# Kernel optimization log

Hardware: AMD Instinct MI355X
Metric: run time of the kernel (lower is better)

## Reference

```python
import jax, jax.numpy as jnp
import numpy as np


def setup_inputs() -> dict:
    key = jax.random.key(0)
    B, F, H, W, C_out = 8, 64, 128, 128, 32
    V = H * W                     # grid vertices
    E = 3 * V                     # edges; flattened connectivity has 6V entries -> degree 6
    F2 = F // 2
    dim_channel = 6 * F2          # 192
    mid = dim_channel // 2        # 96
    out_ch = 2 * C_out            # 64
    k1, k2, k3, k4 = jax.random.split(key, 4)
    features = jax.random.normal(k1, (B, F, E), dtype=jnp.float32)
    # each vertex appears exactly 6 times in the flattened connectivity
    conn_flat = jax.random.permutation(k2, jnp.tile(jnp.arange(V, dtype=jnp.int32), 6))
    connectivity = conn_flat.reshape(E, 2)
    W1 = jax.random.normal(k3, (dim_channel, mid), dtype=jnp.float32) / np.sqrt(dim_channel)
    b1 = jnp.zeros((mid,), dtype=jnp.float32)
    W2 = jax.random.normal(k4, (mid, out_ch), dtype=jnp.float32) / np.sqrt(mid)
    b2 = jnp.zeros((out_ch,), dtype=jnp.float32)
    return {"features": features, "connectivity": connectivity,
            "output_dim": (H, W, C_out), "W1": W1, "b1": b1, "W2": W2, "b2": b2}


def _occurrence_rank(edges):
    # occ[i] = number of j < i with edges[j] == edges[i] (matches the serial
    # images_index bookkeeping in the torch loop). Stable argsort groups equal
    # vertices while preserving original order within a group.
    n = edges.shape[0]
    order = jnp.argsort(edges)            # stable by default in jax
    sorted_e = edges[order]
    first = jnp.searchsorted(sorted_e, sorted_e, side='left')
    rank_sorted = (jnp.arange(n) - first).astype(jnp.int32)
    return jnp.zeros(n, dtype=jnp.int32).at[order].set(rank_sorted)


def reference(features, connectivity, output_dim, W1, b1, W2, b2):
    B, F, E = features.shape
    H, Wd, C_out = int(output_dim[0]), int(output_dim[1]), int(output_dim[2])
    V = H * Wd
    F2 = F // 2
    edges = connectivity.reshape(-1)                      # [2E]
    # [B, F, E] -> [B, E, F] -> [B, 2E, F/2]: one half-feature per edge endpoint
    mesh = jnp.transpose(features, (0, 2, 1)).reshape(B, 2 * E, F2)
    occ = _occurrence_rank(edges)                         # slot per endpoint, 0..5
    # scatter half-features into [B, V, 6, F/2]; (vertex, slot) pairs are unique
    img = jnp.zeros((B, V, 6, F2), features.dtype).at[:, edges, occ, :].set(mesh)
    x = img.reshape(B, H, Wd, 6 * F2).transpose(0, 3, 1, 2)   # [B, 6*F/2, H, W]
    # 1x1 ConvTranspose2d == pointwise GEMM (torch weight layout [in, out, 1, 1])
    y = jax.nn.relu(jnp.einsum('bihw,io->bohw', x, W1) + b1[None, :, None, None])
    out = jax.nn.relu(jnp.einsum('bihw,io->bohw', y, W2) + b2[None, :, None, None])
    return out
```

## Files before the change

### kernel.cpp

```cpp
#include <hip/hip_runtime.h>
#include <hip/hip_bf16.h>
#include <stdint.h>

namespace {
constexpr int Bb   = 8;
constexpr int Ff   = 64;
constexpr int Ee   = 49152;
constexpr int Vv   = 16384;
constexpr int F2   = 32;
constexpr int TWOE = 2 * Ee;
constexpr int MID  = 96;
constexpr int OUTC = 64;
}

typedef __attribute__((ext_vector_type(8))) short bf16x8;
typedef __attribute__((ext_vector_type(4))) float f32x4;
typedef __attribute__((ext_vector_type(4))) unsigned int u32x4;

__global__ void prep_misc(const float* __restrict__ W1, const float* __restrict__ W2,
                          __hip_bfloat16* __restrict__ w1f, __hip_bfloat16* __restrict__ w2f,
                          int* __restrict__ cnt) {
    int tid = blockIdx.x * 256 + threadIdx.x;
    if (tid < Vv) cnt[tid] = 0;
    if (tid < 18432) {
        int j = tid & 7, l = (tid >> 3) & 63, ft = tid >> 9;
        int kk = ft / 6, nt = ft - kk * 6;
        int k = kk * 32 + (l >> 4) * 8 + j;
        int n = nt * 16 + (l & 15);
        w1f[tid] = __float2bfloat16(W1[k * MID + n]);
    } else if (tid < 24576) {
        int t2 = tid - 18432;
        int j = t2 & 7, l = (t2 >> 3) & 63, ft = t2 >> 9;
        int kk = ft >> 2, nt = ft & 3;
        int k = kk * 32 + (l >> 4) * 8 + j;
        int n = nt * 16 + (l & 15);
        w2f[t2] = __float2bfloat16(W2[k * OUTC + n]);
    }
}

__global__ void bucket_fill(const int* __restrict__ conn, int* __restrict__ cnt,
                            int* __restrict__ buckets) {
    int i = blockIdx.x * 256 + threadIdx.x;
    if (i >= TWOE) return;
    int v = conn[i];
    int pos = atomicAdd(&cnt[v], 1);
    if (pos < 6) buckets[v * 6 + pos] = i;
}

__global__ void sort6_inv(const int* __restrict__ buckets, int* __restrict__ dest) {
    int v = blockIdx.x * 256 + threadIdx.x;
    if (v >= Vv) return;
    int a[6];
#pragma unroll
    for (int k = 0; k < 6; ++k) a[k] = buckets[v * 6 + k];
#define CSWAP(x, y) { int lo = min(a[x], a[y]); int hi = max(a[x], a[y]); a[x] = lo; a[y] = hi; }
    CSWAP(1, 2) CSWAP(4, 5) CSWAP(0, 2) CSWAP(3, 5) CSWAP(0, 1) CSWAP(3, 4)
    CSWAP(2, 5) CSWAP(0, 3) CSWAP(1, 4) CSWAP(2, 4) CSWAP(1, 3) CSWAP(2, 3)
#undef CSWAP
#pragma unroll
    for (int k = 0; k < 6; ++k) dest[a[k]] = v * 6 + k;
}

__global__ __launch_bounds__(256) void scatter_feats(const float* __restrict__ feat,
                                                     const int* __restrict__ dest,
                                                     ushort* __restrict__ xg) {
    __shared__ float tile[64][65];
    const int b  = blockIdx.y;
    const int e0 = blockIdx.x * 64;
    const int t  = threadIdx.x;
    const float* src = feat + (size_t)b * Ff * Ee;
    const int q  = t & 15;
    const int cb = t >> 4;
#pragma unroll
    for (int k = 0; k < 4; ++k) {
        int c = k * 16 + cb;
        float4 d = *reinterpret_cast<const float4*>(src + (size_t)c * Ee + e0 + q * 4);
        tile[c][q * 4 + 0] = d.x;
        tile[c][q * 4 + 1] = d.y;
        tile[c][q * 4 + 2] = d.z;
        tile[c][q * 4 + 3] = d.w;
    }
    __syncthreads();
    ushort* dst_base = xg + (size_t)b * ((size_t)Vv * 192);
#pragma unroll
    for (int it = 0; it < 2; ++it) {
        int item = it * 256 + t;
        int le = item >> 2, s2 = item & 3;
        int e = le >> 1, h = le & 1;
        int i = e0 * 2 + e * 2 + h;
        int d = dest[i];
        int c0 = h * 32 + s2 * 8;
        union { ushort u[8]; u32x4 qv; } pk;
#pragma unroll
        for (int k = 0; k < 8; ++k) {
            __hip_bfloat16 hv = __float2bfloat16(tile[c0 + k][e]);
            pk.u[k] = *reinterpret_cast<ushort*>(&hv);
        }
        __builtin_nontemporal_store(pk.qv,
            reinterpret_cast<u32x4*>(dst_base + (size_t)d * 32 + s2 * 8));
    }
}

__global__ __launch_bounds__(256) void decode_mfma(
    const ushort* __restrict__ xg,
    const __hip_bfloat16* __restrict__ w1f, const float* __restrict__ b1,
    const __hip_bfloat16* __restrict__ w2f, const float* __restrict__ b2,
    float* __restrict__ out)
{
    __shared__ __align__(16) __hip_bfloat16 ys[64][104];
    const int t   = threadIdx.x;
    const int l   = t & 63;
    const int wid = t >> 6;
    const int b   = blockIdx.y;
    const int v0  = blockIdx.x * 64 + wid * 16;
    const int lr  = l & 15;
    const int lg  = l >> 4;

    const ushort* xv = xg + ((size_t)b * Vv + v0) * 192;

    f32x4 acc[6];
#pragma unroll
    for (int nt = 0; nt < 6; ++nt) {
        float bv = b1[nt * 16 + lr];
        acc[nt] = (f32x4){bv, bv, bv, bv};
    }
#pragma unroll
    for (int kk = 0; kk < 6; ++kk) {
        bf16x8 a = *reinterpret_cast<const bf16x8*>(xv + (size_t)lr * 192 + kk * 32 + lg * 8);
#pragma unroll
        for (int nt = 0; nt < 6; ++nt) {
            bf16x8 w = *reinterpret_cast<const bf16x8*>(w1f + ((size_t)((kk * 6 + nt) * 64 + l) * 8));
            acc[nt] = __builtin_amdgcn_mfma_f32_16x16x32_bf16(a, w, acc[nt], 0, 0, 0);
        }
    }
#pragma unroll
    for (int nt = 0; nt < 6; ++nt) {
#pragma unroll
        for (int r = 0; r < 4; ++r) {
            ys[wid * 16 + lg * 4 + r][nt * 16 + lr] = __float2bfloat16(fmaxf(acc[nt][r], 0.0f));
        }
    }
    __syncthreads();

    f32x4 acc2[4];
#pragma unroll
    for (int nt = 0; nt < 4; ++nt) {
        float bv = b2[nt * 16 + lr];
        acc2[nt] = (f32x4){bv, bv, bv, bv};
    }
#pragma unroll
    for (int kk = 0; kk < 3; ++kk) {
        bf16x8 a = *reinterpret_cast<const bf16x8*>(&ys[wid * 16 + lr][kk * 32 + lg * 8]);
#pragma unroll
        for (int nt = 0; nt < 4; ++nt) {
            bf16x8 w = *reinterpret_cast<const bf16x8*>(w2f + ((size_t)((kk * 4 + nt) * 64 + l) * 8));
            acc2[nt] = __builtin_amdgcn_mfma_f32_16x16x32_bf16(a, w, acc2[nt], 0, 0, 0);
        }
    }

    const int vbase = v0 + lg * 4;
#pragma unroll
    for (int nt = 0; nt < 4; ++nt) {
        f32x4 o4;
#pragma unroll
        for (int r = 0; r < 4; ++r) o4[r] = fmaxf(acc2[nt][r], 0.0f);
        __builtin_nontemporal_store(o4,
            reinterpret_cast<f32x4*>(out + (((size_t)(b * OUTC + nt * 16 + lr)) << 14) + vbase));
    }
}

extern "C" void kernel_launch(void* const* d_in, const int* in_sizes, int n_in,
                              void* d_out, int out_size, void* d_ws, size_t ws_size,
                              hipStream_t stream) {
    const float* feat = (const float*)d_in[0];
    const int*   conn = (const int*)d_in[1];
    const float* W1   = (const float*)d_in[3];
    const float* b1   = (const float*)d_in[4];
    const float* W2   = (const float*)d_in[5];
    const float* b2   = (const float*)d_in[6];
    float* out = (float*)d_out;

    char* ws = (char*)d_ws;
    int* cnt     = (int*)ws;
    int* buckets = (int*)(ws + 65536);
    int* dest    = (int*)(ws + 65536 + 393216);
    __hip_bfloat16* w1f = (__hip_bfloat16*)(ws + 65536 + 2 * 393216);
    __hip_bfloat16* w2f = w1f + 18432;
    ushort* xg = (ushort*)(ws + 65536 + 2 * 393216 + 49152);

    prep_misc<<<96, 256, 0, stream>>>(W1, W2, w1f, w2f, cnt);
    bucket_fill<<<(TWOE + 255) / 256, 256, 0, stream>>>(conn, cnt, buckets);
    sort6_inv<<<(Vv + 255) / 256, 256, 0, stream>>>(buckets, dest);
    scatter_feats<<<dim3(Ee / 64, Bb), 256, 0, stream>>>(feat, dest, xg);
    decode_mfma<<<dim3(Vv / 64, Bb), 256, 0, stream>>>(xg, w1f, b1, w2f, b2, out);
}
```

Measured before the change: 74.09 us.

## Interleave batch dimension in intermediate layout so scatter writes contiguous per-slot rows

The intermediate bf16 buffer is reorganised from [B][V][192] to [V][6 slots][B][32], so each scattered endpoint writes one contiguous 512-byte row covering all 8 batches instead of scattered 64-byte pieces. The scatter kernel now handles 16 edges across all batches per block, converting to bf16 before staging in shared memory. The decode kernel reads the new layout with a strided batch offset and uses a flattened 1D grid. This trades coalesced global reads per batch for fewer, larger random writes. The decode loads become 64-byte chunks strided across vertices, which may reduce their locality.

```diff
diff --git a/kernel.cpp b/kernel.cpp
--- a/kernel.cpp
+++ b/kernel.cpp
@@ -7,7 +7,6 @@
 constexpr int Ff   = 64;
 constexpr int Ee   = 49152;
 constexpr int Vv   = 16384;
-constexpr int F2   = 32;
 constexpr int TWOE = 2 * Ee;
 constexpr int MID  = 96;
 constexpr int OUTC = 64;
@@ -64,40 +63,34 @@
 __global__ __launch_bounds__(256) void scatter_feats(const float* __restrict__ feat,
                                                      const int* __restrict__ dest,
                                                      ushort* __restrict__ xg) {
-    __shared__ float tile[64][65];
-    const int b  = blockIdx.y;
-    const int e0 = blockIdx.x * 64;
+    __shared__ __align__(16) ushort tile[16 * 648];
     const int t  = threadIdx.x;
-    const float* src = feat + (size_t)b * Ff * Ee;
-    const int q  = t & 15;
-    const int cb = t >> 4;
+    const int e0 = blockIdx.x * 16;
+    const int c  = t >> 2;
+    const int l4 = t & 3;
+    const int hc = c >> 5, cc = c & 31;
 #pragma unroll
-    for (int k = 0; k < 4; ++k) {
-        int c = k * 16 + cb;
-        float4 d = *reinterpret_cast<const float4*>(src + (size_t)c * Ee + e0 + q * 4);
-        tile[c][q * 4 + 0] = d.x;
-        tile[c][q * 4 + 1] = d.y;
-        tile[c][q * 4 + 2] = d.z;
-        tile[c][q * 4 + 3] = d.w;
+    for (int b = 0; b < 8; ++b) {
+        float4 d = *reinterpret_cast<const float4*>(feat + ((size_t)b * Ff + c) * Ee + e0 + l4 * 4);
+        int base = b * 80 + hc * 40 + cc;
+        float vals[4] = {d.x, d.y, d.z, d.w};
+#pragma unroll
+        for (int j = 0; j < 4; ++j) {
+            __hip_bfloat16 hv = __float2bfloat16(vals[j]);
+            tile[(l4 * 4 + j) * 648 + base] = *reinterpret_cast<ushort*>(&hv);
+        }
     }
     __syncthreads();
-    ushort* dst_base = xg + (size_t)b * ((size_t)Vv * 192);
+    const int ie = t >> 3;
+    const int b  = t & 7;
+    const int e  = ie >> 1, hh = ie & 1;
+    const int d  = dest[e0 * 2 + ie];
+    const ushort* srcl = &tile[e * 648 + b * 80 + hh * 40];
+    ushort* dst = xg + ((size_t)d * 8 + b) * 32;
 #pragma unroll
-    for (int it = 0; it < 2; ++it) {
-        int item = it * 256 + t;
-        int le = item >> 2, s2 = item & 3;
-        int e = le >> 1, h = le & 1;
-        int i = e0 * 2 + e * 2 + h;
-        int d = dest[i];
-        int c0 = h * 32 + s2 * 8;
-        union { ushort u[8]; u32x4 qv; } pk;
-#pragma unroll
-        for (int k = 0; k < 8; ++k) {
-            __hip_bfloat16 hv = __float2bfloat16(tile[c0 + k][e]);
-            pk.u[k] = *reinterpret_cast<ushort*>(&hv);
-        }
-        __builtin_nontemporal_store(pk.qv,
-            reinterpret_cast<u32x4*>(dst_base + (size_t)d * 32 + s2 * 8));
+    for (int j = 0; j < 4; ++j) {
+        u32x4 q = *reinterpret_cast<const u32x4*>(srcl + j * 8);
+        __builtin_nontemporal_store(q, reinterpret_cast<u32x4*>(dst + j * 8));
     }
 }
 
@@ -108,15 +101,16 @@
     float* __restrict__ out)
 {
     __shared__ __align__(16) __hip_bfloat16 ys[64][104];
-    const int t   = threadIdx.x;
-    const int l   = t & 63;
-    const int wid = t >> 6;
-    const int b   = blockIdx.y;
-    const int v0  = blockIdx.x * 64 + wid * 16;
-    const int lr  = l & 15;
-    const int lg  = l >> 4;
+    const int t    = threadIdx.x;
+    const int l    = t & 63;
+    const int wid  = t >> 6;
+    const int bx   = blockIdx.x;
+    const int b    = bx >> 8;
+    const int v0   = (bx & 255) * 64 + wid * 16;
+    const int lr   = l & 15;
+    const int lg   = l >> 4;
 
-    const ushort* xv = xg + ((size_t)b * Vv + v0) * 192;
+    const ushort* xvb = xg + ((size_t)(v0 + lr) * 48 + b) * 32;
 
     f32x4 acc[6];
 #pragma unroll
@@ -126,7 +120,7 @@
     }
 #pragma unroll
     for (int kk = 0; kk < 6; ++kk) {
-        bf16x8 a = *reinterpret_cast<const bf16x8*>(xv + (size_t)lr * 192 + kk * 32 + lg * 8);
+        bf16x8 a = *reinterpret_cast<const bf16x8*>(xvb + kk * 256 + lg * 8);
 #pragma unroll
         for (int nt = 0; nt < 6; ++nt) {
             bf16x8 w = *reinterpret_cast<const bf16x8*>(w1f + ((size_t)((kk * 6 + nt) * 64 + l) * 8));
@@ -191,6 +185,6 @@
     prep_misc<<<96, 256, 0, stream>>>(W1, W2, w1f, w2f, cnt);
     bucket_fill<<<(TWOE + 255) / 256, 256, 0, stream>>>(conn, cnt, buckets);
     sort6_inv<<<(Vv + 255) / 256, 256, 0, stream>>>(buckets, dest);
-    scatter_feats<<<dim3(Ee / 64, Bb), 256, 0, stream>>>(feat, dest, xg);
-    decode_mfma<<<dim3(Vv / 64, Bb), 256, 0, stream>>>(xg, w1f, b1, w2f, b2, out);
+    scatter_feats<<<Ee / 16, 256, 0, stream>>>(feat, dest, xg);
+    decode_mfma<<<2048, 256, 0, stream>>>(xg, w1f, b1, w2f, b2, out);
 }
```

New measurement: 130.8 us. 76.5% more time.
